# Optimization experiments

Measured on AMD Instinct MI355X. Metric: run time of the kernel, lower is better.

Reference implementation:

```python
import jax, jax.numpy as jnp
import numpy as np

B, T, C = 4, 2048, 1024
H = 16
HD = C // H  # head_dim = 64


def setup_inputs() -> dict:
    key = jax.random.key(0)
    k1, k2, k3 = jax.random.split(key, 3)
    x = jax.random.normal(k1, (B, T, C), dtype=jnp.float32)
    # nn.Linear weights stored as (out_features, in_features); y = x @ W.T
    w_qkv = jax.random.normal(k2, (3 * C, C), dtype=jnp.float32) * (1.0 / np.sqrt(C))
    w_out = jax.random.normal(k3, (C, C), dtype=jnp.float32) * (1.0 / np.sqrt(C))
    return {"x": x, "w_qkv": w_qkv, "w_out": w_out}


def reference(x, w_qkv, w_out):
    Bb, Tt, Cc = x.shape
    qkv = jnp.einsum('btc,oc->bto', x, w_qkv)  # (B,T,3C)
    q, k, v = jnp.split(qkv, 3, axis=2)
    # (B,T,H,HD) -> (B,H,T,HD)
    q = q.reshape(Bb, Tt, H, HD).transpose(0, 2, 1, 3)
    k = k.reshape(Bb, Tt, H, HD).transpose(0, 2, 1, 3)
    v = v.reshape(Bb, Tt, H, HD).transpose(0, 2, 1, 3)
    scores = jnp.einsum('bhqd,bhkd->bhqk', q, k) / jnp.sqrt(jnp.float32(HD))
    causal = jnp.tril(jnp.ones((Tt, Tt), dtype=bool))  # True = keep
    scores = jnp.where(causal[None, None], scores, jnp.float32(-jnp.inf))
    weights = jax.nn.softmax(scores, axis=-1)
    att = jnp.einsum('bhqk,bhkd->bhqd', weights, v)  # (B,H,T,HD)
    att = att.transpose(0, 2, 1, 3).reshape(Bb, Tt, Cc)
    return jnp.einsum('btc,oc->bto', att, w_out)
```

## Files before the change

### kernel.cpp

```cpp
#include <hip/hip_runtime.h>
#include <hip/hip_bf16.h>

#define B_   4
#define T_   2048
#define C_   1024
#define H_   16
#define HD_  64
#define M_   8192
#define N1_  3072
#define N2_  1024

typedef __attribute__((ext_vector_type(8))) short bf16x8;
typedef __attribute__((ext_vector_type(4))) float f32x4;

static __device__ __forceinline__ unsigned short f2bf(float f) {
  union { float f; unsigned u; } cv; cv.f = f;
  unsigned u = cv.u;
  return (unsigned short)((u + 0x7FFFu + ((u >> 16) & 1u)) >> 16);
}

static __device__ __forceinline__ float exp2_fast(float x) {
  float r;
  asm("v_exp_f32 %0, %1" : "=v"(r) : "v"(x));
  return r;
}

static __device__ __forceinline__ unsigned cvt_pk_bf16(float lo, float hi) {
  unsigned r;
  asm("v_cvt_pk_bf16_f32 %0, %1, %2" : "=v"(r) : "v"(lo), "v"(hi));
  return r;
}

#define AS1 __attribute__((address_space(1)))
#define AS3 __attribute__((address_space(3)))
static __device__ __forceinline__ void gload_lds16(const void* g, void* l) {
  __builtin_amdgcn_global_load_lds((const AS1 void*)g, (AS3 void*)l, 16, 0, 0);
}

#define N4_X  (M_ * C_ / 4)
#define N4_WQ (N1_ * C_ / 4)
#define N4_WO (N2_ * C_ / 4)
__global__ void cast_all_kernel(const float* __restrict__ x, const float* __restrict__ wq,
                                const float* __restrict__ wo,
                                unsigned short* __restrict__ xb, unsigned short* __restrict__ wqb,
                                unsigned short* __restrict__ wob) {
  int stride = gridDim.x * blockDim.x;
  for (int i = blockIdx.x * blockDim.x + threadIdx.x; i < N4_X + N4_WQ + N4_WO; i += stride) {
    const float* src; unsigned short* dst; int j;
    if (i < N4_X)            { src = x;  dst = xb;  j = i; }
    else if (i < N4_X + N4_WQ) { src = wq; dst = wqb; j = i - N4_X; }
    else                     { src = wo; dst = wob; j = i - N4_X - N4_WQ; }
    f32x4 v = ((const f32x4*)src)[j];
    ushort4 o;
    o.x = f2bf(v[0]); o.y = f2bf(v[1]); o.z = f2bf(v[2]); o.w = f2bf(v[3]);
    ((ushort4*)dst)[j] = o;
  }
}

__global__ __launch_bounds__(256, 3) void gemm_qkv(
    const unsigned short* __restrict__ Xb,
    const unsigned short* __restrict__ Wb,
    unsigned short* __restrict__ Qb,
    unsigned short* __restrict__ Kb,
    unsigned short* __restrict__ Vtb)
{
  __shared__ __align__(16) unsigned short As[3][128 * 32];
  __shared__ __align__(16) unsigned short Bs[3][128 * 32];
  const int tid  = threadIdx.x;
  const int lane = tid & 63;
  const int wave = tid >> 6;
  const int wr = wave >> 1, wc = wave & 1;
  const int g = lane >> 4, q4 = lane & 15;
  const int row0 = blockIdx.x * 128;
  const int col0 = blockIdx.y * 128;
  const int NT = C_ / 32;

  auto stage = [&](int kt) {
    const int buf = kt % 3;
    const int k0 = kt * 32;
    #pragma unroll
    for (int i = 0; i < 2; ++i) {
      int cb = wave * 128 + i * 64;
      int c  = cb + lane;
      int r  = c >> 2;
      int j  = (c & 3) ^ ((r >> 1) & 3);
      gload_lds16(Xb + (size_t)(row0 + r) * C_ + k0 + j * 8, (char*)As[buf] + cb * 16);
      gload_lds16(Wb + (size_t)(col0 + r) * C_ + k0 + j * 8, (char*)Bs[buf] + cb * 16);
    }
  };

  f32x4 zero = {0.f, 0.f, 0.f, 0.f};
  f32x4 acc[4][4];
  for (int i = 0; i < 4; ++i) for (int j = 0; j < 4; ++j) acc[i][j] = zero;

  auto ktile = [&](int buf) {
    bf16x8 a[4], b[4];
    #pragma unroll
    for (int im = 0; im < 4; ++im) {
      int row = wr * 64 + im * 16 + q4;
      a[im] = *(const bf16x8*)((const char*)As[buf] + row * 64 + ((g ^ ((row >> 1) & 3)) * 16));
    }
    #pragma unroll
    for (int in_ = 0; in_ < 4; ++in_) {
      int row = wc * 64 + in_ * 16 + q4;
      b[in_] = *(const bf16x8*)((const char*)Bs[buf] + row * 64 + ((g ^ ((row >> 1) & 3)) * 16));
    }
    __builtin_amdgcn_s_setprio(1);
    #pragma unroll
    for (int im = 0; im < 4; ++im)
      #pragma unroll
      for (int in_ = 0; in_ < 4; ++in_)
        acc[im][in_] = __builtin_amdgcn_mfma_f32_16x16x32_bf16(a[im], b[in_], acc[im][in_], 0, 0, 0);
    __builtin_amdgcn_s_setprio(0);
  };

  stage(0); stage(1);
  for (int kt = 0; kt < NT - 1; ++kt) {
    asm volatile("s_waitcnt vmcnt(4)" ::: "memory");
    __builtin_amdgcn_s_barrier();
    __builtin_amdgcn_sched_barrier(0);
    if (kt + 2 < NT) stage(kt + 2);
    ktile(kt % 3);
  }
  asm volatile("s_waitcnt vmcnt(0)" ::: "memory");
  __builtin_amdgcn_s_barrier();
  __builtin_amdgcn_sched_barrier(0);
  ktile((NT - 1) % 3);

  const float SC = 0.125f * 1.44269504f;
  #pragma unroll
  for (int im = 0; im < 4; ++im) {
    #pragma unroll
    for (int in_ = 0; in_ < 4; ++in_) {
      f32x4 v = acc[im][in_];
      int col = col0 + wc * 64 + in_ * 16 + q4;
      int which = col >> 10;
      int cc = col & 1023;
      int h = cc >> 6, d = cc & 63;
      int r0 = row0 + wr * 64 + im * 16 + g * 4;
      int bb = r0 >> 11, t0 = r0 & 2047;
      if (which == 2) {
        uint2 pk;
        pk.x = cvt_pk_bf16(v[0], v[1]);
        pk.y = cvt_pk_bf16(v[2], v[3]);
        *(uint2*)(Vtb + (((size_t)(bb * 16 + h)) * 64 + d) * T_ + t0) = pk;
      } else {
        unsigned short* dst = (which == 0) ? Qb : Kb;
        float sc = (which == 0) ? SC : 1.f;
        #pragma unroll
        for (int rg = 0; rg < 4; ++rg)
          dst[(((size_t)(bb * 16 + h)) * T_ + t0 + rg) * 64 + d] = f2bf(v[rg] * sc);
      }
    }
  }
}

__global__ __launch_bounds__(256, 3) void attn_kernel(
    const unsigned short* __restrict__ Qb,
    const unsigned short* __restrict__ Kb,
    const unsigned short* __restrict__ Vtb,
    unsigned short* __restrict__ Ob)
{
  __shared__ __align__(16) unsigned short Ks[2][64 * 64];
  __shared__ __align__(16) unsigned short Vs[2][64 * 64];
  __shared__ __align__(16) unsigned short Ps[4][32 * 64];
  const int tid  = threadIdx.x;
  const int lane = tid & 63;
  const int wave = tid >> 6;
  const int g = lane >> 4, q4 = lane & 15;
  const int bh = blockIdx.x;
  const int qt = 15 - blockIdx.y;
  const unsigned short* Qp = Qb  + (size_t)bh * T_ * 64;
  const unsigned short* Kp = Kb  + (size_t)bh * T_ * 64;
  const unsigned short* Vp = Vtb + (size_t)bh * 64 * T_;
  const int qb = qt * 128 + wave * 32;
  const int nT = 2 * qt + 2;
  const int nKeys = qb + 31;

  bf16x8 qf[2][2];
  #pragma unroll
  for (int qtl = 0; qtl < 2; ++qtl)
    #pragma unroll
    for (int ks = 0; ks < 2; ++ks)
      qf[qtl][ks] = *(const bf16x8*)(Qp + (size_t)(qb + qtl * 16 + q4) * 64 + ks * 32 + g * 8);

  bf16x8 ones;
  #pragma unroll
  for (int i = 0; i < 8; ++i) ones[i] = (short)0x3F80;

  f32x4 zero = {0.f, 0.f, 0.f, 0.f};
  f32x4 oacc[2][4], lacc[2];
  #pragma unroll
  for (int i = 0; i < 2; ++i) {
    lacc[i] = zero;
    #pragma unroll
    for (int jj = 0; jj < 4; ++jj) oacc[i][jj] = zero;
  }

  auto stage = [&](int t, int buf) {
    const int kv0 = t * 64;
    #pragma unroll
    for (int i = 0; i < 2; ++i) {
      int cb = wave * 128 + i * 64;
      int c  = cb + lane;
      int r  = c >> 3;
      int jx = (c & 7) ^ (r & 7);
      gload_lds16(Kp + (size_t)(kv0 + r) * 64 + jx * 8, (char*)Ks[buf] + cb * 16);
      gload_lds16(Vp + (size_t)r * T_ + kv0 + jx * 8,   (char*)Vs[buf] + cb * 16);
    }
  };

  stage(0, 0);
  for (int t = 0; t < nT; ++t) {
    asm volatile("s_waitcnt vmcnt(0)" ::: "memory");
    __builtin_amdgcn_s_barrier();
    __builtin_amdgcn_sched_barrier(0);
    if (t + 1 < nT) stage(t + 1, (t + 1) & 1);
    const int cur = t & 1;
    const int kv0 = t * 64;
    if (kv0 > nKeys) continue;

    f32x4 s[4][2];
    #pragma unroll
    for (int mt = 0; mt < 4; ++mt)
      #pragma unroll
      for (int qtl = 0; qtl < 2; ++qtl) s[mt][qtl] = zero;
    #pragma unroll
    for (int ks = 0; ks < 2; ++ks) {
      bf16x8 kf[4];
      #pragma unroll
      for (int mt = 0; mt < 4; ++mt) {
        int row = mt * 16 + q4;
        int byte = (row * 128 + (ks * 32 + g * 8) * 2) ^ ((row & 7) << 4);
        kf[mt] = *(const bf16x8*)((const char*)Ks[cur] + byte);
      }
      __builtin_amdgcn_s_setprio(1);
      #pragma unroll
      for (int mt = 0; mt < 4; ++mt)
        #pragma unroll
        for (int qtl = 0; qtl < 2; ++qtl)
          s[mt][qtl] = __builtin_amdgcn_mfma_f32_16x16x32_bf16(kf[mt], qf[qtl][ks], s[mt][qtl], 0, 0, 0);
      __builtin_amdgcn_s_setprio(0);
    }

    const bool needMask = (kv0 + 63 > qb);
    if (needMask) {
      #pragma unroll
      for (int mt = 0; mt < 4; ++mt)
        #pragma unroll
        for (int qtl = 0; qtl < 2; ++qtl)
          #pragma unroll
          for (int rg = 0; rg < 4; ++rg) {
            int key = kv0 + mt * 16 + g * 4 + rg;
            int qrow = qb + qtl * 16 + q4;
            s[mt][qtl][rg] = (key <= qrow) ? s[mt][qtl][rg] : -1e30f;
          }
    }
    #pragma unroll
    for (int qtl = 0; qtl < 2; ++qtl)
      #pragma unroll
      for (int mt = 0; mt < 4; ++mt) {
        float p0 = exp2_fast(s[mt][qtl][0]);
        float p1 = exp2_fast(s[mt][qtl][1]);
        float p2 = exp2_fast(s[mt][qtl][2]);
        float p3 = exp2_fast(s[mt][qtl][3]);
        uint2 pk;
        pk.x = cvt_pk_bf16(p0, p1);
        pk.y = cvt_pk_bf16(p2, p3);
        int row = qtl * 16 + q4;
        int byte = (row * 128 + (mt * 16 + g * 4) * 2) ^ ((row & 7) << 4);
        *(uint2*)((char*)Ps[wave] + byte) = pk;
      }
    #pragma unroll
    for (int ks = 0; ks < 2; ++ks) {
      bf16x8 pf[2], vf[4];
      #pragma unroll
      for (int qtl = 0; qtl < 2; ++qtl) {
        int row = qtl * 16 + q4;
        int byte = (row * 128 + (ks * 32 + g * 8) * 2) ^ ((row & 7) << 4);
        pf[qtl] = *(const bf16x8*)((const char*)Ps[wave] + byte);
      }
      #pragma unroll
      for (int dt = 0; dt < 4; ++dt) {
        int row = dt * 16 + q4;
        int byte = (row * 128 + (ks * 32 + g * 8) * 2) ^ ((row & 7) << 4);
        vf[dt] = *(const bf16x8*)((const char*)Vs[cur] + byte);
      }
      __builtin_amdgcn_s_setprio(1);
      #pragma unroll
      for (int qtl = 0; qtl < 2; ++qtl) {
        #pragma unroll
        for (int dt = 0; dt < 4; ++dt)
          oacc[qtl][dt] = __builtin_amdgcn_mfma_f32_16x16x32_bf16(pf[qtl], vf[dt], oacc[qtl][dt], 0, 0, 0);
        lacc[qtl] = __builtin_amdgcn_mfma_f32_16x16x32_bf16(pf[qtl], ones, lacc[qtl], 0, 0, 0);
      }
      __builtin_amdgcn_s_setprio(0);
    }
  }

  #pragma unroll
  for (int qtl = 0; qtl < 2; ++qtl) {
    #pragma unroll
    for (int dt = 0; dt < 4; ++dt) {
      #pragma unroll
      for (int rg = 0; rg < 4; ++rg) {
        int tq = qb + qtl * 16 + g * 4 + rg;
        int d = dt * 16 + q4;
        Ob[((size_t)bh * T_ + tq) * 64 + d] = f2bf(oacc[qtl][dt][rg] / lacc[qtl][rg]);
      }
    }
  }
}

__global__ __launch_bounds__(256, 3) void gemm_out(
    const unsigned short* __restrict__ Ob,
    const unsigned short* __restrict__ Wo,
    float* __restrict__ Out)
{
  __shared__ __align__(16) unsigned short As[3][128 * 32];
  __shared__ __align__(16) unsigned short Bs[3][128 * 32];
  const int tid  = threadIdx.x;
  const int lane = tid & 63;
  const int wave = tid >> 6;
  const int wr = wave >> 1, wc = wave & 1;
  const int g = lane >> 4, q4 = lane & 15;
  const int row0 = blockIdx.x * 128;
  const int col0 = blockIdx.y * 128;
  const int NT = C_ / 32;

  auto stage = [&](int kt) {
    const int buf = kt % 3;
    const int k0 = kt * 32;
    #pragma unroll
    for (int i = 0; i < 2; ++i) {
      int cb = wave * 128 + i * 64;
      int c  = cb + lane;
      int r  = c >> 2;
      int j  = (c & 3) ^ ((r >> 1) & 3);
      int rr = row0 + r;
      int cc = k0 + j * 8;
      const unsigned short* srcA =
          Ob + (((size_t)((rr >> 11) * 16 + (cc >> 6))) * T_ + (rr & 2047)) * 64 + (cc & 63);
      gload_lds16(srcA, (char*)As[buf] + cb * 16);
      gload_lds16(Wo + (size_t)(col0 + r) * C_ + cc, (char*)Bs[buf] + cb * 16);
    }
  };

  f32x4 zero = {0.f, 0.f, 0.f, 0.f};
  f32x4 acc[4][4];
  for (int i = 0; i < 4; ++i) for (int j = 0; j < 4; ++j) acc[i][j] = zero;

  auto ktile = [&](int buf) {
    bf16x8 a[4], b[4];
    #pragma unroll
    for (int im = 0; im < 4; ++im) {
      int row = wr * 64 + im * 16 + q4;
      a[im] = *(const bf16x8*)((const char*)As[buf] + row * 64 + ((g ^ ((row >> 1) & 3)) * 16));
    }
    #pragma unroll
    for (int in_ = 0; in_ < 4; ++in_) {
      int row = wc * 64 + in_ * 16 + q4;
      b[in_] = *(const bf16x8*)((const char*)Bs[buf] + row * 64 + ((g ^ ((row >> 1) & 3)) * 16));
    }
    __builtin_amdgcn_s_setprio(1);
    #pragma unroll
    for (int im = 0; im < 4; ++im)
      #pragma unroll
      for (int in_ = 0; in_ < 4; ++in_)
        acc[im][in_] = __builtin_amdgcn_mfma_f32_16x16x32_bf16(a[im], b[in_], acc[im][in_], 0, 0, 0);
    __builtin_amdgcn_s_setprio(0);
  };

  stage(0); stage(1);
  for (int kt = 0; kt < NT - 1; ++kt) {
    asm volatile("s_waitcnt vmcnt(4)" ::: "memory");
    __builtin_amdgcn_s_barrier();
    __builtin_amdgcn_sched_barrier(0);
    if (kt + 2 < NT) stage(kt + 2);
    ktile(kt % 3);
  }
  asm volatile("s_waitcnt vmcnt(0)" ::: "memory");
  __builtin_amdgcn_s_barrier();
  __builtin_amdgcn_sched_barrier(0);
  ktile((NT - 1) % 3);

  #pragma unroll
  for (int im = 0; im < 4; ++im)
    #pragma unroll
    for (int in_ = 0; in_ < 4; ++in_) {
      int col = col0 + wc * 64 + in_ * 16 + q4;
      #pragma unroll
      for (int rg = 0; rg < 4; ++rg) {
        int r = row0 + wr * 64 + im * 16 + g * 4 + rg;
        Out[(size_t)r * C_ + col] = acc[im][in_][rg];
      }
    }
}

extern "C" void kernel_launch(void* const* d_in, const int* in_sizes, int n_in,
                              void* d_out, int out_size, void* d_ws, size_t ws_size,
                              hipStream_t stream) {
  const float* x     = (const float*)d_in[0];
  const float* w_qkv = (const float*)d_in[1];
  const float* w_out = (const float*)d_in[2];
  float* out = (float*)d_out;
  char* ws = (char*)d_ws;
  unsigned short* xb  = (unsigned short*)(ws);
  unsigned short* wqb = (unsigned short*)(ws + 16777216);
  unsigned short* wob = (unsigned short*)(ws + 16777216 + 6291456);
  unsigned short* Qb  = (unsigned short*)(ws + 25165824);
  unsigned short* Kb  = (unsigned short*)(ws + 25165824 + 16777216);
  unsigned short* Vtb = (unsigned short*)(ws + 25165824 + 2 * 16777216);
  unsigned short* Ob  = (unsigned short*)(ws + 25165824 + 3 * 16777216);

  cast_all_kernel<<<2048, 256, 0, stream>>>(x, w_qkv, w_out, xb, wqb, wob);
  gemm_qkv<<<dim3(M_ / 128, N1_ / 128), 256, 0, stream>>>(xb, wqb, Qb, Kb, Vtb);
  attn_kernel<<<dim3(B_ * H_, 16), 256, 0, stream>>>(Qb, Kb, Vtb, Ob);
  gemm_out<<<dim3(M_ / 128, N2_ / 128), 256, 0, stream>>>(Ob, wob, out);
}
```

Baseline: 153.1 us.

## Replace P LDS staging with lane shuffles, reorder query tiles, raise occupancy

Removes the per-wave shared-memory buffer for the softmax probabilities and rebuilds the MFMA A-operand fragments with cross-lane shuffles from packed bf16 registers. Query-tile indices are permuted so that heavy and light causal tiles are interleaved across the grid, and launch bounds request 4 blocks per CU instead of 3. The intent is to cut LDS traffic and footprint, raise occupancy and balance causal workload. In exchange it adds 16 ds_bpermute shuffles plus selects per key tile and more register pressure under the tighter bound.

```diff
diff --git a/kernel.cpp b/kernel.cpp
--- a/kernel.cpp
+++ b/kernel.cpp
@@ -155,7 +155,7 @@
   }
 }
 
-__global__ __launch_bounds__(256, 3) void attn_kernel(
+__global__ __launch_bounds__(256, 4) void attn_kernel(
     const unsigned short* __restrict__ Qb,
     const unsigned short* __restrict__ Kb,
     const unsigned short* __restrict__ Vtb,
@@ -163,19 +163,23 @@
 {
   __shared__ __align__(16) unsigned short Ks[2][64 * 64];
   __shared__ __align__(16) unsigned short Vs[2][64 * 64];
-  __shared__ __align__(16) unsigned short Ps[4][32 * 64];
   const int tid  = threadIdx.x;
   const int lane = tid & 63;
   const int wave = tid >> 6;
   const int g = lane >> 4, q4 = lane & 15;
   const int bh = blockIdx.x;
-  const int qt = 15 - blockIdx.y;
+  const int yy = blockIdx.y, rr_ = yy >> 2, kk_ = yy & 3;
+  const int qt = (rr_ == 0) ? 15 - 2 * kk_ : (rr_ == 1) ? 2 * kk_
+               : (rr_ == 2) ? 14 - 2 * kk_ : 1 + 2 * kk_;
   const unsigned short* Qp = Qb  + (size_t)bh * T_ * 64;
   const unsigned short* Kp = Kb  + (size_t)bh * T_ * 64;
   const unsigned short* Vp = Vtb + (size_t)bh * 64 * T_;
   const int qb = qt * 128 + wave * 32;
   const int nT = 2 * qt + 2;
   const int nKeys = qb + 31;
+  const int i0 = ((g & 1) * 2) * 16 + q4;
+  const int i1 = i0 + 16;
+  const bool hi_half = (lane >= 32);
 
   bf16x8 qf[2][2];
   #pragma unroll
@@ -220,65 +224,67 @@
     const int kv0 = t * 64;
     if (kv0 > nKeys) continue;
 
-    f32x4 s[4][2];
-    #pragma unroll
-    for (int mt = 0; mt < 4; ++mt)
-      #pragma unroll
-      for (int qtl = 0; qtl < 2; ++qtl) s[mt][qtl] = zero;
-    #pragma unroll
-    for (int ks = 0; ks < 2; ++ks) {
-      bf16x8 kf[4];
-      #pragma unroll
-      for (int mt = 0; mt < 4; ++mt) {
-        int row = mt * 16 + q4;
-        int byte = (row * 128 + (ks * 32 + g * 8) * 2) ^ ((row & 7) << 4);
-        kf[mt] = *(const bf16x8*)((const char*)Ks[cur] + byte);
-      }
-      __builtin_amdgcn_s_setprio(1);
-      #pragma unroll
-      for (int mt = 0; mt < 4; ++mt)
+    const bool needMask = (kv0 + 63 > qb);
+    unsigned pw0[2][4], pw1[2][4];
+    #pragma unroll
+    for (int qtl = 0; qtl < 2; ++qtl) {
+      f32x4 s4[4];
+      #pragma unroll
+      for (int mt = 0; mt < 4; ++mt) s4[mt] = zero;
+      #pragma unroll
+      for (int ks = 0; ks < 2; ++ks) {
+        bf16x8 kf[4];
         #pragma unroll
-        for (int qtl = 0; qtl < 2; ++qtl)
-          s[mt][qtl] = __builtin_amdgcn_mfma_f32_16x16x32_bf16(kf[mt], qf[qtl][ks], s[mt][qtl], 0, 0, 0);
-      __builtin_amdgcn_s_setprio(0);
-    }
-
-    const bool needMask = (kv0 + 63 > qb);
-    if (needMask) {
-      #pragma unroll
-      for (int mt = 0; mt < 4; ++mt)
+        for (int mt = 0; mt < 4; ++mt) {
+          int row = mt * 16 + q4;
+          int byte = (row * 128 + (ks * 32 + g * 8) * 2) ^ ((row & 7) << 4);
+          kf[mt] = *(const bf16x8*)((const char*)Ks[cur] + byte);
+        }
+        __builtin_amdgcn_s_setprio(1);
         #pragma unroll
-        for (int qtl = 0; qtl < 2; ++qtl)
+        for (int mt = 0; mt < 4; ++mt)
+          s4[mt] = __builtin_amdgcn_mfma_f32_16x16x32_bf16(kf[mt], qf[qtl][ks], s4[mt], 0, 0, 0);
+        __builtin_amdgcn_s_setprio(0);
+      }
+      if (needMask) {
+        #pragma unroll
+        for (int mt = 0; mt < 4; ++mt)
           #pragma unroll
           for (int rg = 0; rg < 4; ++rg) {
             int key = kv0 + mt * 16 + g * 4 + rg;
             int qrow = qb + qtl * 16 + q4;
-            s[mt][qtl][rg] = (key <= qrow) ? s[mt][qtl][rg] : -1e30f;
+            s4[mt][rg] = (key <= qrow) ? s4[mt][rg] : -1e30f;
           }
-    }
-    #pragma unroll
-    for (int qtl = 0; qtl < 2; ++qtl)
+      }
       #pragma unroll
       for (int mt = 0; mt < 4; ++mt) {
-        float p0 = exp2_fast(s[mt][qtl][0]);
-        float p1 = exp2_fast(s[mt][qtl][1]);
-        float p2 = exp2_fast(s[mt][qtl][2]);
-        float p3 = exp2_fast(s[mt][qtl][3]);
-        uint2 pk;
-        pk.x = cvt_pk_bf16(p0, p1);
-        pk.y = cvt_pk_bf16(p2, p3);
-        int row = qtl * 16 + q4;
-        int byte = (row * 128 + (mt * 16 + g * 4) * 2) ^ ((row & 7) << 4);
-        *(uint2*)((char*)Ps[wave] + byte) = pk;
-      }
+        float p0 = exp2_fast(s4[mt][0]);
+        float p1 = exp2_fast(s4[mt][1]);
+        float p2 = exp2_fast(s4[mt][2]);
+        float p3 = exp2_fast(s4[mt][3]);
+        pw0[qtl][mt] = cvt_pk_bf16(p0, p1);
+        pw1[qtl][mt] = cvt_pk_bf16(p2, p3);
+      }
+    }
     #pragma unroll
     for (int ks = 0; ks < 2; ++ks) {
       bf16x8 pf[2], vf[4];
       #pragma unroll
       for (int qtl = 0; qtl < 2; ++qtl) {
-        int row = qtl * 16 + q4;
-        int byte = (row * 128 + (ks * 32 + g * 8) * 2) ^ ((row & 7) << 4);
-        pf[qtl] = *(const bf16x8*)((const char*)Ps[wave] + byte);
+        int a_lo = __shfl((int)pw0[qtl][2 * ks],     i0);
+        int a_hi = __shfl((int)pw0[qtl][2 * ks + 1], i0);
+        int b_lo = __shfl((int)pw1[qtl][2 * ks],     i0);
+        int b_hi = __shfl((int)pw1[qtl][2 * ks + 1], i0);
+        int c_lo = __shfl((int)pw0[qtl][2 * ks],     i1);
+        int c_hi = __shfl((int)pw0[qtl][2 * ks + 1], i1);
+        int e_lo = __shfl((int)pw1[qtl][2 * ks],     i1);
+        int e_hi = __shfl((int)pw1[qtl][2 * ks + 1], i1);
+        union { int i[4]; bf16x8 v; } u;
+        u.i[0] = hi_half ? a_hi : a_lo;
+        u.i[1] = hi_half ? b_hi : b_lo;
+        u.i[2] = hi_half ? c_hi : c_lo;
+        u.i[3] = hi_half ? e_hi : e_lo;
+        pf[qtl] = u.v;
       }
       #pragma unroll
       for (int dt = 0; dt < 4; ++dt) {
```

After: 190.0 us. 24.1% more time.
